# Optimization experiments

Hardware: AMD Instinct MI355X
Metric: run time of the kernel (lower is better)

The kernel has to match this reference:

```python
import jax, jax.numpy as jnp
import numpy as np

B, C, H, W = 32, 256, 64, 64
M, D = 256, 512           # memory_size, memory_dim
NH, HD = 8, 64            # heads, head_dim
EPS = 1e-5


def setup_inputs() -> dict:
    key = jax.random.key(0)
    ks = jax.random.split(key, 12)
    s = 0.02
    return {
        "x": jax.random.normal(ks[0], (B, C, H, W), jnp.float32),
        "memory_bank": jax.random.normal(ks[1], (M, D), jnp.float32),
        "enc_conv_w": jax.random.normal(ks[2], (D // 2, C), jnp.float32) * s,  # 1x1 conv == channel matmul
        "enc_conv_b": jnp.zeros((D // 2,), jnp.float32),
        "bn_gamma": jnp.ones((D // 2,), jnp.float32),
        "bn_beta": jnp.zeros((D // 2,), jnp.float32),
        "bn_mean": jnp.zeros((D // 2,), jnp.float32),
        "bn_var": jnp.ones((D // 2,), jnp.float32),
        "enc_lin_w": jax.random.normal(ks[3], (D, D // 2), jnp.float32) * s,
        "enc_lin_b": jnp.zeros((D,), jnp.float32),
        "ln_gamma": jnp.ones((D,), jnp.float32),
        "ln_beta": jnp.zeros((D,), jnp.float32),
        "attn_in_w": jax.random.normal(ks[4], (3 * D, D), jnp.float32) * s,
        "attn_in_b": jnp.zeros((3 * D,), jnp.float32),
        "attn_out_w": jax.random.normal(ks[5], (D, D), jnp.float32) * s,
        "attn_out_b": jnp.zeros((D,), jnp.float32),
        "gate_w": jax.random.normal(ks[6], (D, 2 * D), jnp.float32) * s,
        "gate_b": jnp.zeros((D,), jnp.float32),
        "rec_w1": jax.random.normal(ks[7], (D // 2, D), jnp.float32) * s,
        "rec_b1": jnp.zeros((D // 2,), jnp.float32),
        "rec_w2": jax.random.normal(ks[8], (C, D // 2), jnp.float32) * s,
        "rec_b2": jnp.zeros((C,), jnp.float32),
        "spat_conv_w": jax.random.normal(ks[9], (1, 2, 7, 7), jnp.float32) * s,
    }


def reference(x, memory_bank, enc_conv_w, enc_conv_b, bn_gamma, bn_beta, bn_mean, bn_var,
              enc_lin_w, enc_lin_b, ln_gamma, ln_beta, attn_in_w, attn_in_b,
              attn_out_w, attn_out_b, gate_w, gate_b, rec_w1, rec_b1, rec_w2, rec_b2,
              spat_conv_w):
    # ---- feature encoder: 1x1 conv -> BN(eval) -> ReLU -> global avg pool -> Linear -> LayerNorm ----
    h = jnp.einsum('bchw,oc->bohw', x, enc_conv_w) + enc_conv_b[None, :, None, None]
    bn_scale = (bn_gamma / jnp.sqrt(bn_var + EPS))[None, :, None, None]
    h = (h - bn_mean[None, :, None, None]) * bn_scale + bn_beta[None, :, None, None]
    h = jax.nn.relu(h)
    h = h.mean(axis=(2, 3))                                   # (B, D//2)
    h = h @ enc_lin_w.T + enc_lin_b                           # (B, D)
    mu = h.mean(-1, keepdims=True)
    var = h.var(-1, keepdims=True)
    enc = (h - mu) / jnp.sqrt(var + EPS) * ln_gamma + ln_beta  # (B, D)

    # ---- memory retrieval: MHA with q_len=1, keys/values = shared memory bank ----
    Wq, Wk, Wv = jnp.split(attn_in_w, 3, axis=0)
    bq, bk, bv = jnp.split(attn_in_b, 3)
    q = (enc @ Wq.T + bq).reshape(B, NH, HD)                  # (B, H, d)
    k = (memory_bank @ Wk.T + bk).reshape(M, NH, HD)          # (M, H, d) — batch-shared
    v = (memory_bank @ Wv.T + bv).reshape(M, NH, HD)
    scores = jnp.einsum('bhd,mhd->bhm', q, k) / np.float32(np.sqrt(HD))
    att = jax.nn.softmax(scores, axis=-1)                     # (B, H, M)
    ctx = jnp.einsum('bhm,mhd->bhd', att, v).reshape(B, D)
    retrieved = ctx @ attn_out_w.T + attn_out_b               # (B, D)

    # ---- gated fusion ----
    gate = jax.nn.sigmoid(jnp.concatenate([enc, retrieved], axis=-1) @ gate_w.T + gate_b)
    fused = gate * enc + (1.0 - gate) * retrieved             # (B, D)

    # ---- per-channel weights from fused features ----
    sw = jax.nn.sigmoid(jax.nn.relu(fused @ rec_w1.T + rec_b1) @ rec_w2.T + rec_b2)  # (B, C)

    # ---- spatial attention on [avg, max] channel stats ----
    avg = x.mean(axis=1, keepdims=True)
    mx = x.max(axis=1, keepdims=True)
    sp_in = jnp.concatenate([avg, mx], axis=1)                # (B, 2, H, W)
    sa = jax.lax.conv_general_dilated(sp_in, spat_conv_w, (1, 1), [(3, 3), (3, 3)],
                                      dimension_numbers=('NCHW', 'OIHW', 'NCHW'))
    sa = jax.nn.sigmoid(sa)                                   # (B, 1, H, W)

    return x * sw[:, :, None, None] * sa                      # (B, C, H, W)
```

## Files before the change

### kernel.cpp

```cpp
#include <hip/hip_runtime.h>
#include <math.h>

#define EPSV 1e-5f

typedef __attribute__((ext_vector_type(8))) short short8;
typedef __attribute__((ext_vector_type(8))) unsigned short ushort8;
typedef __attribute__((ext_vector_type(4))) float f32x4;

__device__ __forceinline__ unsigned short f2bf(float f){
  unsigned u = __builtin_bit_cast(unsigned, f);
  u += 0x7fffu + ((u >> 16) & 1u);
  return (unsigned short)(u >> 16);
}
__device__ __forceinline__ float dot4f(float4 w, const float* v){
  return w.x*v[0] + w.y*v[1] + w.z*v[2] + w.w*v[3];
}
__device__ __forceinline__ float sigmoidf(float v){ return 1.f/(1.f + expf(-v)); }

__global__ __launch_bounds__(256) void k_pack(const float* __restrict__ w1,
                                              const float* __restrict__ wattn,
                                              unsigned short* __restrict__ p1,
                                              unsigned short* __restrict__ pkv){
  const int total1 = 256*256, total2 = 1024*512;
  for (int idx = blockIdx.x*256 + threadIdx.x; idx < total1 + total2; idx += gridDim.x*256){
    if (idx < total1){
      int o = idx >> 8, c = idx & 255;
      int off = (((o>>4)*8 + (c>>5))*64 + (((c>>3)&3)*16 + (o&15)))*8 + (c&7);
      p1[off] = f2bf(w1[idx]);
    } else {
      int j = idx - total1; int o = j >> 9, c = j & 511;
      int off = (((o>>4)*16 + (c>>5))*64 + (((c>>3)&3)*16 + (o&15)))*8 + (c&7);
      pkv[off] = f2bf(wattn[512*512 + j]);
    }
  }
}

__global__ __launch_bounds__(256) void k_conv(
    const float* __restrict__ x, const unsigned short* __restrict__ wp,
    const float* __restrict__ cb, const float* __restrict__ bng,
    const float* __restrict__ bnb, const float* __restrict__ bnm,
    const float* __restrict__ bnv,
    float* __restrict__ ppool, float* __restrict__ wavg, float* __restrict__ wmax){
  int bid = blockIdx.x;
  int b = bid >> 6, tile = bid & 63;
  int px0 = tile << 6;
  int t = threadIdx.x;
  int lane = t & 63, wv = t >> 6;
  int px = t & 63, cg = wv;
  __shared__ __align__(16) unsigned short a_lds[16384];
  __shared__ float st_s[256], st_m[256];

  const float* xb = x + (size_t)b*(256*4096) + px0 + px;

  float ssum = 0.f, smax = -3.4e38f;
  const unsigned wbase = (((px >> 4) << 6) + ((unsigned)cg << 4) + (px & 15)) << 4;

  #pragma unroll
  for (int ch = 0; ch < 8; ++ch){
    float xv[8];
    #pragma unroll
    for (int u = 0; u < 8; ++u)
      xv[u] = xb[(size_t)(ch*32 + cg*8 + u) * 4096];
    ushort8 pk;
    #pragma unroll
    for (int u = 0; u < 8; ++u){
      ssum += xv[u];
      smax = fmaxf(smax, xv[u]);
      pk[u] = f2bf(xv[u]);
    }
    *(ushort8*)((char*)a_lds + wbase + (ch << 12)) = pk;
  }
  st_s[t] = ssum; st_m[t] = smax;
  __syncthreads();

  if (t < 64){
    float s = st_s[t] + st_s[t+64] + st_s[t+128] + st_s[t+192];
    float m = fmaxf(fmaxf(st_m[t], st_m[t+64]), fmaxf(st_m[t+128], st_m[t+192]));
    wavg[(b << 12) + px0 + t] = s * (1.f/256.f);
    wmax[(b << 12) + px0 + t] = m;
  }

  f32x4 acc[4][4];
  #pragma unroll
  for (int i = 0; i < 4; ++i)
    #pragma unroll
    for (int j = 0; j < 4; ++j){ f32x4 z = {0.f,0.f,0.f,0.f}; acc[i][j] = z; }

  #pragma unroll
  for (int ch = 0; ch < 8; ++ch){
    short8 afr[4];
    #pragma unroll
    for (int mf = 0; mf < 4; ++mf)
      afr[mf] = *(const short8*)((const char*)a_lds + (ch << 12) + (mf << 10) + lane*16);
    #pragma unroll
    for (int nf = 0; nf < 4; ++nf){
      short8 bfr = *(const short8*)(wp + (size_t)(((wv*4 + nf)*8 + ch) * 512 + lane*8));
      #pragma unroll
      for (int mf = 0; mf < 4; ++mf)
        acc[mf][nf] = __builtin_amdgcn_mfma_f32_16x16x32_bf16(afr[mf], bfr, acc[mf][nf], 0, 0, 0);
    }
  }

  #pragma unroll
  for (int nf = 0; nf < 4; ++nf){
    int o = (wv << 6) + (nf << 4) + (lane & 15);
    float sc = bng[o] * rsqrtf(bnv[o] + EPSV);
    float sh = bnb[o] + (cb[o] - bnm[o]) * sc;
    float ps = 0.f;
    #pragma unroll
    for (int mf = 0; mf < 4; ++mf)
      #pragma unroll
      for (int r = 0; r < 4; ++r)
        ps += fmaxf(acc[mf][nf][r] * sc + sh, 0.f);
    ps += __shfl_xor(ps, 16, 64);
    ps += __shfl_xor(ps, 32, 64);
    if ((lane & 48) == 0)
      ppool[(size_t)((b << 6) + tile)*256 + o] = ps;
  }
}

__global__ __launch_bounds__(256) void k_enc(const float* __restrict__ pp,
    const float* __restrict__ lw, const float* __restrict__ lb,
    const float* __restrict__ lng, const float* __restrict__ lnb,
    float* __restrict__ enc){
  int b = blockIdx.x, t = threadIdx.x;
  __shared__ __align__(16) float p_s[256];
  __shared__ float h_s[512], red[8];
  float s = 0.f;
  for (int tile = 0; tile < 64; ++tile) s += pp[(size_t)((b<<6)+tile)*256 + t];
  p_s[t] = s * (1.f/4096.f);
  __syncthreads();
  float hv[2];
  #pragma unroll
  for (int k = 0; k < 2; ++k){
    int d = t + k*256;
    const float4* wr = (const float4*)(lw + (size_t)d*256);
    float a = 0.f;
    for (int j = 0; j < 64; ++j) a += dot4f(wr[j], &p_s[4*j]);
    hv[k] = a + lb[d];
    h_s[d] = hv[k];
  }
  float ls = hv[0] + hv[1], lq = hv[0]*hv[0] + hv[1]*hv[1];
  #pragma unroll
  for (int msk = 1; msk < 64; msk <<= 1){
    ls += __shfl_xor(ls, msk, 64);
    lq += __shfl_xor(lq, msk, 64);
  }
  if ((t & 63) == 0){ red[t>>6] = ls; red[4 + (t>>6)] = lq; }
  __syncthreads();
  float su = red[0]+red[1]+red[2]+red[3];
  float sq = red[4]+red[5]+red[6]+red[7];
  float mu = su * (1.f/512.f);
  float vr = sq * (1.f/512.f) - mu*mu;
  float rstd = rsqrtf(vr + EPSV);
  #pragma unroll
  for (int k = 0; k < 2; ++k){
    int d = t + k*256;
    enc[(size_t)b*512 + d] = (h_s[d] - mu)*rstd*lng[d] + lnb[d];
  }
}

__global__ __launch_bounds__(256) void k_kv(const float* __restrict__ mb,
    const unsigned short* __restrict__ wp, const float* __restrict__ attb,
    float* __restrict__ kvb){
  int bid = blockIdx.x;
  int mt = bid >> 4, nt = bid & 15;
  int m0 = mt << 4;
  int mu = nt >> 3;
  int ncol0 = (nt & 7) << 6;
  int t = threadIdx.x, lane = t & 63, wv = t >> 6;
  int l15 = lane & 15, l4 = lane >> 4;

  const float* arow = mb + (size_t)(m0 + l15)*512 + l4*8;
  int ofrag = (nt << 2) + wv;

  f32x4 acc = {0.f,0.f,0.f,0.f};
  #pragma unroll
  for (int ch = 0; ch < 16; ++ch){
    float4 a0 = *(const float4*)(arow + ch*32);
    float4 a1 = *(const float4*)(arow + ch*32 + 4);
    short8 afr;
    afr[0] = (short)f2bf(a0.x); afr[1] = (short)f2bf(a0.y);
    afr[2] = (short)f2bf(a0.z); afr[3] = (short)f2bf(a0.w);
    afr[4] = (short)f2bf(a1.x); afr[5] = (short)f2bf(a1.y);
    afr[6] = (short)f2bf(a1.z); afr[7] = (short)f2bf(a1.w);
    short8 bfr = *(const short8*)(wp + (size_t)(ofrag*16 + ch)*512 + lane*8);
    acc = __builtin_amdgcn_mfma_f32_16x16x32_bf16(afr, bfr, acc, 0, 0, 0);
  }
  float bias = attb[512 + mu*512 + ncol0 + (wv << 4) + l15];
  #pragma unroll
  for (int i = 0; i < 4; ++i){
    int row = m0 + l4*4 + i;
    int col = ncol0 + (wv << 4) + l15;
    kvb[(size_t)mu*131072 + (size_t)row*512 + col] = acc[i] + bias;
  }
}

__global__ __launch_bounds__(256) void k_qkattn(const float* __restrict__ enc,
    const float* __restrict__ kvb, const float* __restrict__ attw,
    const float* __restrict__ attb, float* __restrict__ ctxout){
  int bid = blockIdx.x;
  int b = bid >> 3, h = bid & 7;
  int t = threadIdx.x;
  __shared__ float e_s[512];
  __shared__ __align__(16) float q_s[64];
  __shared__ float att_s[256];
  __shared__ float red_s[256];
  __shared__ float r2[8];

  e_s[t]       = enc[(size_t)b*512 + t];
  e_s[t + 256] = enc[(size_t)b*512 + 256 + t];
  __syncthreads();

  {
    int i = t >> 2, part = t & 3;
    const float4* wr = (const float4*)(attw + (size_t)(h*64 + i)*512 + part*128);
    const float* ev = e_s + part*128;
    float a = 0.f;
    #pragma unroll
    for (int j = 0; j < 32; ++j) a += dot4f(wr[j], ev + 4*j);
    a += __shfl_xor(a, 1, 64);
    a += __shfl_xor(a, 2, 64);
    if (part == 0) q_s[i] = a + attb[h*64 + i];
  }
  __syncthreads();

  float sc;
  {
    const float4* kr = (const float4*)(kvb + (size_t)t*512 + h*64);
    const float4* qr = (const float4*)q_s;
    float a = 0.f;
    #pragma unroll
    for (int j = 0; j < 16; ++j){
      float4 kk = kr[j], qq = qr[j];
      a += kk.x*qq.x + kk.y*qq.y + kk.z*qq.z + kk.w*qq.w;
    }
    sc = a * 0.125f;
  }
  int wv = t >> 6, lane = t & 63;
  float mx = sc;
  #pragma unroll
  for (int msk = 1; msk < 64; msk <<= 1) mx = fmaxf(mx, __shfl_xor(mx, msk, 64));
  if (lane == 0) r2[wv] = mx;
  __syncthreads();
  mx = fmaxf(fmaxf(r2[0], r2[1]), fmaxf(r2[2], r2[3]));
  float ex = expf(sc - mx);
  float sum = ex;
  #pragma unroll
  for (int msk = 1; msk < 64; msk <<= 1) sum += __shfl_xor(sum, msk, 64);
  if (lane == 0) r2[4 + wv] = sum;
  __syncthreads();
  float inv = 1.f / (r2[4] + r2[5] + r2[6] + r2[7]);
  att_s[t] = ex * inv;
  __syncthreads();

  {
    const float* vbase = kvb + 131072 + (size_t)(wv*64)*512 + h*64 + lane;
    const float* at = att_s + wv*64;
    float a = 0.f;
    #pragma unroll 8
    for (int m = 0; m < 64; ++m) a += at[m] * vbase[(size_t)m*512];
    red_s[wv*64 + lane] = a;
  }
  __syncthreads();
  if (t < 64)
    ctxout[(size_t)b*512 + h*64 + t] = red_s[t] + red_s[64+t] + red_s[128+t] + red_s[192+t];
}

__global__ __launch_bounds__(256) void k_outproj(const float* __restrict__ ctx,
    const float* __restrict__ ow, const float* __restrict__ obv,
    float* __restrict__ retr){
  int bid = blockIdx.x;
  int b = bid >> 3, n0 = (bid & 7) << 6;
  int t = threadIdx.x;
  __shared__ float c_s[512];
  c_s[t]       = ctx[(size_t)b*512 + t];
  c_s[t + 256] = ctx[(size_t)b*512 + 256 + t];
  __syncthreads();
  int o = n0 + (t >> 2), part = t & 3;
  const float4* wr = (const float4*)(ow + (size_t)o*512 + part*128);
  const float* cv = c_s + part*128;
  float a = 0.f;
  #pragma unroll
  for (int j = 0; j < 32; ++j) a += dot4f(wr[j], cv + 4*j);
  a += __shfl_xor(a, 1, 64);
  a += __shfl_xor(a, 2, 64);
  if (part == 0) retr[(size_t)b*512 + o] = a + obv[o];
}

__global__ __launch_bounds__(256) void k_gate(const float* __restrict__ enc,
    const float* __restrict__ retr, const float* __restrict__ gw,
    const float* __restrict__ gb, float* __restrict__ fused){
  int bid = blockIdx.x;
  int b = bid >> 3, n0 = (bid & 7) << 6;
  int t = threadIdx.x;
  __shared__ float ef[1024];
  ef[t]        = enc[(size_t)b*512 + t];
  ef[t + 256]  = enc[(size_t)b*512 + 256 + t];
  ef[t + 512]  = retr[(size_t)b*512 + t];
  ef[t + 768]  = retr[(size_t)b*512 + 256 + t];
  __syncthreads();
  int o = n0 + (t >> 2), part = t & 3;
  const float4* wr = (const float4*)(gw + (size_t)o*1024 + part*256);
  const float* fv = ef + part*256;
  float a = 0.f;
  #pragma unroll
  for (int j = 0; j < 64; ++j) a += dot4f(wr[j], fv + 4*j);
  a += __shfl_xor(a, 1, 64);
  a += __shfl_xor(a, 2, 64);
  if (part == 0){
    float g = sigmoidf(a + gb[o]);
    fused[(size_t)b*512 + o] = g*ef[o] + (1.f - g)*ef[512 + o];
  }
}

__global__ __launch_bounds__(256) void k_rec1(const float* __restrict__ fused,
    const float* __restrict__ r1w, const float* __restrict__ r1b,
    float* __restrict__ t1){
  int bid = blockIdx.x;
  int b = bid >> 2, n0 = (bid & 3) << 6;
  int t = threadIdx.x;
  __shared__ float f_s[512];
  f_s[t]       = fused[(size_t)b*512 + t];
  f_s[t + 256] = fused[(size_t)b*512 + 256 + t];
  __syncthreads();
  int o = n0 + (t >> 2), part = t & 3;
  const float4* wr = (const float4*)(r1w + (size_t)o*512 + part*128);
  const float* fv = f_s + part*128;
  float a = 0.f;
  #pragma unroll
  for (int j = 0; j < 32; ++j) a += dot4f(wr[j], fv + 4*j);
  a += __shfl_xor(a, 1, 64);
  a += __shfl_xor(a, 2, 64);
  if (part == 0) t1[(size_t)b*256 + o] = fmaxf(a + r1b[o], 0.f);
}

__global__ __launch_bounds__(256) void k_rec2(const float* __restrict__ t1,
    const float* __restrict__ r2w, const float* __restrict__ r2b,
    float* __restrict__ swout){
  int bid = blockIdx.x;
  int b = bid >> 2, n0 = (bid & 3) << 6;
  int t = threadIdx.x;
  __shared__ float t_s[256];
  t_s[t] = t1[(size_t)b*256 + t];
  __syncthreads();
  int o = n0 + (t >> 2), part = t & 3;
  const float4* wr = (const float4*)(r2w + (size_t)o*256 + part*64);
  const float* tv = t_s + part*64;
  float a = 0.f;
  #pragma unroll
  for (int j = 0; j < 16; ++j) a += dot4f(wr[j], tv + 4*j);
  a += __shfl_xor(a, 1, 64);
  a += __shfl_xor(a, 2, 64);
  if (part == 0) swout[(size_t)b*256 + o] = sigmoidf(a + r2b[o]);
}

__global__ __launch_bounds__(256) void k_spconv(const float* __restrict__ wavg,
    const float* __restrict__ wmax, const float* __restrict__ wgt,
    float* __restrict__ sa){
  __shared__ float w_s[98];
  int t = threadIdx.x;
  if (t < 98) w_s[t] = wgt[t];
  __syncthreads();
  int b = blockIdx.x >> 4;
  int px = ((blockIdx.x & 15) << 8) + t;
  int y = px >> 6, xx = px & 63;
  const float* pa = wavg + (b << 12);
  const float* pm = wmax + (b << 12);
  float a = 0.f;
  #pragma unroll
  for (int ky = 0; ky < 7; ++ky){
    int yy = y + ky - 3;
    if (yy < 0 || yy >= 64) continue;
    #pragma unroll
    for (int kx = 0; kx < 7; ++kx){
      int x2 = xx + kx - 3;
      if (x2 < 0 || x2 >= 64) continue;
      int o = (yy << 6) + x2;
      a += pa[o]*w_s[ky*7+kx] + pm[o]*w_s[49+ky*7+kx];
    }
  }
  sa[(b << 12) + px] = sigmoidf(a);
}

__global__ __launch_bounds__(256) void k_final(const float* __restrict__ x,
    const float* __restrict__ sw, const float* __restrict__ sa,
    float* __restrict__ out){
  const size_t total = 8388608;
  for (size_t q = (size_t)blockIdx.x*256 + threadIdx.x; q < total; q += (size_t)gridDim.x*256){
    size_t b = q >> 18;
    int c = (int)((q >> 10) & 255);
    int p4 = (int)(q & 1023);
    float4 xv = ((const float4*)x)[q];
    float4 sv = ((const float4*)sa)[(b << 10) + p4];
    float s = sw[(b << 8) + c];
    float4 o;
    o.x = xv.x * s * sv.x;
    o.y = xv.y * s * sv.y;
    o.z = xv.z * s * sv.z;
    o.w = xv.w * s * sv.w;
    ((float4*)out)[q] = o;
  }
}

extern "C" void kernel_launch(void* const* d_in, const int* in_sizes, int n_in,
                              void* d_out, int out_size, void* d_ws, size_t ws_size,
                              hipStream_t stream){
  const float* x    = (const float*)d_in[0];
  const float* mb   = (const float*)d_in[1];
  const float* w1   = (const float*)d_in[2];
  const float* cbv  = (const float*)d_in[3];
  const float* bng  = (const float*)d_in[4];
  const float* bnb  = (const float*)d_in[5];
  const float* bnm  = (const float*)d_in[6];
  const float* bnv  = (const float*)d_in[7];
  const float* lw   = (const float*)d_in[8];
  const float* lb   = (const float*)d_in[9];
  const float* lng  = (const float*)d_in[10];
  const float* lnb  = (const float*)d_in[11];
  const float* attw = (const float*)d_in[12];
  const float* attb = (const float*)d_in[13];
  const float* ow   = (const float*)d_in[14];
  const float* obv  = (const float*)d_in[15];
  const float* gw   = (const float*)d_in[16];
  const float* gb   = (const float*)d_in[17];
  const float* r1w  = (const float*)d_in[18];
  const float* r1b  = (const float*)d_in[19];
  const float* r2w  = (const float*)d_in[20];
  const float* r2b  = (const float*)d_in[21];
  const float* spw  = (const float*)d_in[22];
  float* out = (float*)d_out;

  char* ws = (char*)d_ws;
  unsigned short* w1p  = (unsigned short*)(ws + 0);
  unsigned short* wkvp = (unsigned short*)(ws + 131072);
  float* ppool = (float*)(ws + 1179648);
  float* wavg  = (float*)(ws + 3276800);
  float* wmax  = (float*)(ws + 3801088);
  float* encb  = (float*)(ws + 4325376);
  float* kvb   = (float*)(ws + 4390912);
  float* swb   = (float*)(ws + 5439488);
  float* sab   = (float*)(ws + 5472256);
  float* ctxb  = (float*)(ws + 5996544);
  float* retrb = (float*)(ws + 6062080);
  float* fusedb= (float*)(ws + 6127616);
  float* t1b   = (float*)(ws + 6193152);

  k_pack   <<<2304, 256, 0, stream>>>(w1, attw, w1p, wkvp);
  k_conv   <<<2048, 256, 0, stream>>>(x, w1p, cbv, bng, bnb, bnm, bnv, ppool, wavg, wmax);
  k_enc    <<<32,   256, 0, stream>>>(ppool, lw, lb, lng, lnb, encb);
  k_kv     <<<256,  256, 0, stream>>>(mb, wkvp, attb, kvb);
  k_qkattn <<<256,  256, 0, stream>>>(encb, kvb, attw, attb, ctxb);
  k_outproj<<<256,  256, 0, stream>>>(ctxb, ow, obv, retrb);
  k_gate   <<<256,  256, 0, stream>>>(encb, retrb, gw, gb, fusedb);
  k_rec1   <<<128,  256, 0, stream>>>(fusedb, r1w, r1b, t1b);
  k_rec2   <<<128,  256, 0, stream>>>(t1b, r2w, r2b, swb);
  k_spconv <<<512,  256, 0, stream>>>(wavg, wmax, spw, sab);
  k_final  <<<2048, 256, 0, stream>>>(x, swb, sab, out);
}
```

Measured before the change: 179.3 us.

## Restructure conv GEMM with larger tiles, double-buffered LDS and prefetched loads

The 1x1-conv kernel now processes 256 pixels per block with 512 threads arranged as a 2x4 wave grid, instead of 64 pixels per 256-thread block. The channel dimension is streamed in 32-channel chunks through a double-buffered, XOR-swizzled LDS stage, and the next chunk's float4 global loads are issued before the MFMAs on the current chunk. This is meant to overlap global loads with matrix math, widen loads to float4, and reduce LDS bank conflicts and the number of partial pools. In exchange it uses more registers per thread (32 accumulator tiles) and launches only 512 blocks, which may lower occupancy. The partial-pool count per batch falls from 64 to 16, and the encoder reduction is updated to match.

```diff
diff --git a/kernel.cpp b/kernel.cpp
--- a/kernel.cpp
+++ b/kernel.cpp
@@ -5,6 +5,7 @@
 
 typedef __attribute__((ext_vector_type(8))) short short8;
 typedef __attribute__((ext_vector_type(8))) unsigned short ushort8;
+typedef __attribute__((ext_vector_type(4))) unsigned short ushort4v;
 typedef __attribute__((ext_vector_type(4))) float f32x4;
 
 __device__ __forceinline__ unsigned short f2bf(float f){
@@ -35,88 +36,116 @@
   }
 }
 
-__global__ __launch_bounds__(256) void k_conv(
+__global__ __launch_bounds__(512, 2) void k_conv(
     const float* __restrict__ x, const unsigned short* __restrict__ wp,
     const float* __restrict__ cb, const float* __restrict__ bng,
     const float* __restrict__ bnb, const float* __restrict__ bnm,
     const float* __restrict__ bnv,
     float* __restrict__ ppool, float* __restrict__ wavg, float* __restrict__ wmax){
   int bid = blockIdx.x;
-  int b = bid >> 6, tile = bid & 63;
-  int px0 = tile << 6;
+  int b = bid >> 4, tile = bid & 15;
+  int px0 = tile << 8;
   int t = threadIdx.x;
   int lane = t & 63, wv = t >> 6;
-  int px = t & 63, cg = wv;
-  __shared__ __align__(16) unsigned short a_lds[16384];
-  __shared__ float st_s[256], st_m[256];
-
-  const float* xb = x + (size_t)b*(256*4096) + px0 + px;
-
-  float ssum = 0.f, smax = -3.4e38f;
-  const unsigned wbase = (((px >> 4) << 6) + ((unsigned)cg << 4) + (px & 15)) << 4;
-
-  #pragma unroll
-  for (int ch = 0; ch < 8; ++ch){
-    float xv[8];
-    #pragma unroll
-    for (int u = 0; u < 8; ++u)
-      xv[u] = xb[(size_t)(ch*32 + cg*8 + u) * 4096];
-    ushort8 pk;
-    #pragma unroll
-    for (int u = 0; u < 8; ++u){
-      ssum += xv[u];
-      smax = fmaxf(smax, xv[u]);
-      pk[u] = f2bf(xv[u]);
-    }
-    *(ushort8*)((char*)a_lds + wbase + (ch << 12)) = pk;
-  }
-  st_s[t] = ssum; st_m[t] = smax;
-  __syncthreads();
-
-  if (t < 64){
-    float s = st_s[t] + st_s[t+64] + st_s[t+128] + st_s[t+192];
-    float m = fmaxf(fmaxf(st_m[t], st_m[t+64]), fmaxf(st_m[t+128], st_m[t+192]));
+  int wm = wv >> 2, wn = wv & 3;
+
+  __shared__ __align__(16) unsigned short a_lds[2][8192];
+  __shared__ float st_s[8][256];
+  __shared__ float sm_s[8][256];
+  __shared__ float pr_s[2][256];
+
+  const float* xb = x + (size_t)b*(256*4096) + px0;
+
+  float ss[4] = {0.f,0.f,0.f,0.f};
+  float smx[4] = {-3.4e38f,-3.4e38f,-3.4e38f,-3.4e38f};
+
+  f32x4 acc[8][4];
+  #pragma unroll
+  for (int m = 0; m < 8; ++m)
+    #pragma unroll
+    for (int n = 0; n < 4; ++n){ f32x4 z = {0.f,0.f,0.f,0.f}; acc[m][n] = z; }
+
+  unsigned wb[4];
+  const int g = (wv >> 1) & 3, jh = wv & 1;
+  #pragma unroll
+  for (int i = 0; i < 4; ++i){
+    int px = 4*lane + i;
+    unsigned byte = (unsigned)((px >> 6) << 12) + ((unsigned)((px >> 4) & 3) << 10)
+                  + ((unsigned)g << 8) + ((unsigned)(px & 15) << 4) + ((unsigned)jh << 3);
+    wb[i] = byte ^ (((unsigned)(px >> 4) & 7u) << 4);
+  }
+
+  float4 ld[4];
+  #pragma unroll
+  for (int q = 0; q < 4; ++q)
+    ld[q] = *(const float4*)(xb + (size_t)(wv*4 + q)*4096 + lane*4);
+
+  for (int kc = 0; kc < 8; ++kc){
+    if (kc > 0) __syncthreads();
+    char* stg = (char*)a_lds[kc & 1];
+    #pragma unroll
+    for (int i = 0; i < 4; ++i){
+      float v0 = ld[0][i], v1 = ld[1][i], v2 = ld[2][i], v3 = ld[3][i];
+      ss[i] += (v0 + v1) + (v2 + v3);
+      smx[i] = fmaxf(fmaxf(smx[i], fmaxf(v0, v1)), fmaxf(v2, v3));
+      ushort4v pk;
+      pk[0] = f2bf(v0); pk[1] = f2bf(v1); pk[2] = f2bf(v2); pk[3] = f2bf(v3);
+      *(ushort4v*)(stg + wb[i]) = pk;
+    }
+    if (kc < 7){
+      #pragma unroll
+      for (int q = 0; q < 4; ++q)
+        ld[q] = *(const float4*)(xb + (size_t)((kc+1)*32 + wv*4 + q)*4096 + lane*4);
+    }
+    __syncthreads();
+    const char* rd = (const char*)a_lds[kc & 1];
+    short8 afr[8];
+    #pragma unroll
+    for (int m = 0; m < 8; ++m){
+      int pxb = wm*128 + m*16;
+      unsigned byte = (unsigned)((pxb >> 6) << 12) + ((unsigned)(m & 3) << 10)
+                    + ((unsigned)(lane >> 4) << 8) + ((unsigned)(lane & 15) << 4);
+      afr[m] = *(const short8*)(rd + (byte ^ ((unsigned)(m & 7) << 4)));
+    }
+    #pragma unroll
+    for (int nf = 0; nf < 4; ++nf){
+      short8 bfr = *(const short8*)(wp + (size_t)(((wn*4 + nf)*8 + kc) * 512 + lane*8));
+      #pragma unroll
+      for (int m = 0; m < 8; ++m)
+        acc[m][nf] = __builtin_amdgcn_mfma_f32_16x16x32_bf16(afr[m], bfr, acc[m][nf], 0, 0, 0);
+    }
+  }
+
+  *(float4*)&st_s[wv][4*lane] = *(float4*)ss;
+  *(float4*)&sm_s[wv][4*lane] = *(float4*)smx;
+  __syncthreads();
+  if (t < 256){
+    float s = 0.f, m = -3.4e38f;
+    #pragma unroll
+    for (int w = 0; w < 8; ++w){ s += st_s[w][t]; m = fmaxf(m, sm_s[w][t]); }
     wavg[(b << 12) + px0 + t] = s * (1.f/256.f);
     wmax[(b << 12) + px0 + t] = m;
   }
 
-  f32x4 acc[4][4];
-  #pragma unroll
-  for (int i = 0; i < 4; ++i)
-    #pragma unroll
-    for (int j = 0; j < 4; ++j){ f32x4 z = {0.f,0.f,0.f,0.f}; acc[i][j] = z; }
-
-  #pragma unroll
-  for (int ch = 0; ch < 8; ++ch){
-    short8 afr[4];
-    #pragma unroll
-    for (int mf = 0; mf < 4; ++mf)
-      afr[mf] = *(const short8*)((const char*)a_lds + (ch << 12) + (mf << 10) + lane*16);
-    #pragma unroll
-    for (int nf = 0; nf < 4; ++nf){
-      short8 bfr = *(const short8*)(wp + (size_t)(((wv*4 + nf)*8 + ch) * 512 + lane*8));
-      #pragma unroll
-      for (int mf = 0; mf < 4; ++mf)
-        acc[mf][nf] = __builtin_amdgcn_mfma_f32_16x16x32_bf16(afr[mf], bfr, acc[mf][nf], 0, 0, 0);
-    }
-  }
-
   #pragma unroll
   for (int nf = 0; nf < 4; ++nf){
-    int o = (wv << 6) + (nf << 4) + (lane & 15);
+    int o = (wn << 6) + (nf << 4) + (lane & 15);
     float sc = bng[o] * rsqrtf(bnv[o] + EPSV);
     float sh = bnb[o] + (cb[o] - bnm[o]) * sc;
     float ps = 0.f;
     #pragma unroll
-    for (int mf = 0; mf < 4; ++mf)
+    for (int m = 0; m < 8; ++m)
       #pragma unroll
       for (int r = 0; r < 4; ++r)
-        ps += fmaxf(acc[mf][nf][r] * sc + sh, 0.f);
+        ps += fmaxf(acc[m][nf][r] * sc + sh, 0.f);
     ps += __shfl_xor(ps, 16, 64);
     ps += __shfl_xor(ps, 32, 64);
     if ((lane & 48) == 0)
-      ppool[(size_t)((b << 6) + tile)*256 + o] = ps;
-  }
+      pr_s[wm][(wn << 6) + (nf << 4) + lane] = ps;
+  }
+  __syncthreads();
+  if (t < 256)
+    ppool[(size_t)((b << 4) + tile)*256 + t] = pr_s[0][t] + pr_s[1][t];
 }
 
 __global__ __launch_bounds__(256) void k_enc(const float* __restrict__ pp,
@@ -127,7 +156,7 @@
   __shared__ __align__(16) float p_s[256];
   __shared__ float h_s[512], red[8];
   float s = 0.f;
-  for (int tile = 0; tile < 64; ++tile) s += pp[(size_t)((b<<6)+tile)*256 + t];
+  for (int tile = 0; tile < 16; ++tile) s += pp[(size_t)((b<<4)+tile)*256 + t];
   p_s[t] = s * (1.f/4096.f);
   __syncthreads();
   float hv[2];
@@ -447,7 +476,7 @@
   float* t1b   = (float*)(ws + 6193152);
 
   k_pack   <<<2304, 256, 0, stream>>>(w1, attw, w1p, wkvp);
-  k_conv   <<<2048, 256, 0, stream>>>(x, w1p, cbv, bng, bnb, bnm, bnv, ppool, wavg, wmax);
+  k_conv   <<<512,  512, 0, stream>>>(x, w1p, cbv, bng, bnb, bnm, bnv, ppool, wavg, wmax);
   k_enc    <<<32,   256, 0, stream>>>(ppool, lw, lb, lng, lnb, encb);
   k_kv     <<<256,  256, 0, stream>>>(mb, wkvp, attb, kvb);
   k_qkattn <<<256,  256, 0, stream>>>(encb, kvb, attw, attb, ctxb);
```

Result: no change. 181.9 us (median of 4 runs) (+1.4%).

## Split conv into bf16 transpose pass and larger-tile MFMA GEMM kernel

Applied to the files above, without the earlier changes.

Replaces the fused conv kernel, which read x with channel-strided scalar loads, with two kernels. The first converts x to bf16 and writes it in an MFMA-fragment layout using coalesced float4 loads and an LDS transpose. The second is a 512-thread GEMM over 128-pixel tiles that computes the avg/max channel stats from the bf16 copy and reduces the partial pools in LDS, halving the ppool entries. This adds an extra round trip through global memory for a 64 MB bf16 intermediate. The spatial stats are now computed from bf16-rounded values, so avg and max lose some precision.

```diff
diff --git a/kernel.cpp b/kernel.cpp
--- a/kernel.cpp
+++ b/kernel.cpp
@@ -11,6 +11,9 @@
   unsigned u = __builtin_bit_cast(unsigned, f);
   u += 0x7fffu + ((u >> 16) & 1u);
   return (unsigned short)(u >> 16);
+}
+__device__ __forceinline__ float bf2f(unsigned short u){
+  return __builtin_bit_cast(float, ((unsigned)u) << 16);
 }
 __device__ __forceinline__ float dot4f(float4 w, const float* v){
   return w.x*v[0] + w.y*v[1] + w.z*v[2] + w.w*v[3];
@@ -35,50 +38,61 @@
   }
 }
 
-__global__ __launch_bounds__(256) void k_conv(
-    const float* __restrict__ x, const unsigned short* __restrict__ wp,
+__global__ __launch_bounds__(512) void k_xpose(const float* __restrict__ x,
+                                               unsigned short* __restrict__ xa){
+  int bid = blockIdx.x;
+  int b = bid >> 5, cg = bid & 31;
+  int t = threadIdx.x;
+  __shared__ unsigned int lds[12288];
+  const float* base = x + (size_t)b*1048576 + (size_t)cg*32768;
+  unsigned short* xab = xa + (size_t)b*1048576;
+
+  for (int half = 0; half < 2; ++half){
+    if (half) __syncthreads();
+    int px0 = half*2048;
+    #pragma unroll
+    for (int u = 0; u < 4; ++u){
+      float4 a = *(const float4*)(base + (size_t)(2*u)*4096 + px0 + 4*t);
+      float4 c = *(const float4*)(base + (size_t)(2*u+1)*4096 + px0 + 4*t);
+      float av[4] = {a.x, a.y, a.z, a.w};
+      float cv[4] = {c.x, c.y, c.z, c.w};
+      #pragma unroll
+      for (int i = 0; i < 4; ++i)
+        lds[(4*t + i)*6 + u] = (unsigned)f2bf(av[i]) | ((unsigned)f2bf(cv[i]) << 16);
+    }
+    __syncthreads();
+    #pragma unroll
+    for (int k = 0; k < 4; ++k){
+      int p = k*512 + t;
+      int PX = px0 + p;
+      uint2 q0 = *(const uint2*)(&lds[p*6]);
+      uint2 q1 = *(const uint2*)(&lds[p*6 + 2]);
+      uint4 val; val.x = q0.x; val.y = q0.y; val.z = q1.x; val.w = q1.y;
+      size_t off = ((size_t)((PX >> 8)*128 + (cg >> 2)*16 + ((PX >> 4) & 15)) << 9)
+                 + ((unsigned)(cg & 3) << 7) + ((unsigned)(PX & 15) << 3);
+      *(uint4*)(xab + off) = val;
+    }
+  }
+}
+
+__global__ __launch_bounds__(512, 4) void k_gemm(
+    const unsigned short* __restrict__ xa, const unsigned short* __restrict__ wp,
     const float* __restrict__ cb, const float* __restrict__ bng,
     const float* __restrict__ bnb, const float* __restrict__ bnm,
     const float* __restrict__ bnv,
     float* __restrict__ ppool, float* __restrict__ wavg, float* __restrict__ wmax){
   int bid = blockIdx.x;
-  int b = bid >> 6, tile = bid & 63;
-  int px0 = tile << 6;
-  int t = threadIdx.x;
-  int lane = t & 63, wv = t >> 6;
-  int px = t & 63, cg = wv;
+  int b = bid >> 5, pt2 = bid & 31;
+  int pt = pt2 >> 1, half = pt2 & 1;
+  int t = threadIdx.x, lane = t & 63, wv = t >> 6;
+  int wm = wv >> 2, wn = wv & 3;
   __shared__ __align__(16) unsigned short a_lds[16384];
-  __shared__ float st_s[256], st_m[256];
-
-  const float* xb = x + (size_t)b*(256*4096) + px0 + px;
-
+  __shared__ float pr_s[2][256];
+
+  const unsigned short* src = xa + (size_t)b*1048576 + (size_t)pt*65536
+                                 + (size_t)half*4096;
+  int px = t >> 2, q = t & 3;
   float ssum = 0.f, smax = -3.4e38f;
-  const unsigned wbase = (((px >> 4) << 6) + ((unsigned)cg << 4) + (px & 15)) << 4;
-
-  #pragma unroll
-  for (int ch = 0; ch < 8; ++ch){
-    float xv[8];
-    #pragma unroll
-    for (int u = 0; u < 8; ++u)
-      xv[u] = xb[(size_t)(ch*32 + cg*8 + u) * 4096];
-    ushort8 pk;
-    #pragma unroll
-    for (int u = 0; u < 8; ++u){
-      ssum += xv[u];
-      smax = fmaxf(smax, xv[u]);
-      pk[u] = f2bf(xv[u]);
-    }
-    *(ushort8*)((char*)a_lds + wbase + (ch << 12)) = pk;
-  }
-  st_s[t] = ssum; st_m[t] = smax;
-  __syncthreads();
-
-  if (t < 64){
-    float s = st_s[t] + st_s[t+64] + st_s[t+128] + st_s[t+192];
-    float m = fmaxf(fmaxf(st_m[t], st_m[t+64]), fmaxf(st_m[t+128], st_m[t+192]));
-    wavg[(b << 12) + px0 + t] = s * (1.f/256.f);
-    wmax[(b << 12) + px0 + t] = m;
-  }
 
   f32x4 acc[4][4];
   #pragma unroll
@@ -86,24 +100,53 @@
     #pragma unroll
     for (int j = 0; j < 4; ++j){ f32x4 z = {0.f,0.f,0.f,0.f}; acc[i][j] = z; }
 
-  #pragma unroll
-  for (int ch = 0; ch < 8; ++ch){
-    short8 afr[4];
-    #pragma unroll
-    for (int mf = 0; mf < 4; ++mf)
-      afr[mf] = *(const short8*)((const char*)a_lds + (ch << 12) + (mf << 10) + lane*16);
-    #pragma unroll
-    for (int nf = 0; nf < 4; ++nf){
-      short8 bfr = *(const short8*)(wp + (size_t)(((wv*4 + nf)*8 + ch) * 512 + lane*8));
+  for (int s = 0; s < 2; ++s){
+    if (s) __syncthreads();
+    #pragma unroll
+    for (int r = 0; r < 4; ++r){
+      ushort8 v = *(const ushort8*)(src + (size_t)(s*4 + r)*8192 + t*8);
+      *(ushort8*)(a_lds + r*4096 + t*8) = v;
+    }
+    __syncthreads();
+    #pragma unroll
+    for (int c = 0; c < 4; ++c){
+      ushort8 sv = *(const ushort8*)(a_lds + ((c*8 + (px >> 4)) << 9)
+                                           + ((q*16 + (px & 15)) << 3));
+      #pragma unroll
+      for (int j = 0; j < 8; ++j){
+        float f = bf2f(sv[j]);
+        ssum += f; smax = fmaxf(smax, f);
+      }
+    }
+    #pragma unroll
+    for (int kcl = 0; kcl < 4; ++kcl){
+      short8 afr[4];
       #pragma unroll
       for (int mf = 0; mf < 4; ++mf)
-        acc[mf][nf] = __builtin_amdgcn_mfma_f32_16x16x32_bf16(afr[mf], bfr, acc[mf][nf], 0, 0, 0);
-    }
+        afr[mf] = *(const short8*)(a_lds + ((kcl*8 + wm*4 + mf) << 9) + lane*8);
+      #pragma unroll
+      for (int nf = 0; nf < 4; ++nf){
+        short8 bfr = *(const short8*)(wp + (size_t)(((wn*4 + nf)*8 + s*4 + kcl)*512) + lane*8);
+        #pragma unroll
+        for (int mf = 0; mf < 4; ++mf)
+          acc[mf][nf] = __builtin_amdgcn_mfma_f32_16x16x32_bf16(afr[mf], bfr, acc[mf][nf], 0, 0, 0);
+      }
+    }
+  }
+
+  ssum += __shfl_xor(ssum, 1, 64);
+  ssum += __shfl_xor(ssum, 2, 64);
+  smax = fmaxf(smax, __shfl_xor(smax, 1, 64));
+  smax = fmaxf(smax, __shfl_xor(smax, 2, 64));
+  if (q == 0){
+    int PX = pt2*128 + px;
+    wavg[(b << 12) + PX] = ssum * (1.f/256.f);
+    wmax[(b << 12) + PX] = smax;
   }
 
   #pragma unroll
   for (int nf = 0; nf < 4; ++nf){
-    int o = (wv << 6) + (nf << 4) + (lane & 15);
+    int o = (wn << 6) + (nf << 4) + (lane & 15);
     float sc = bng[o] * rsqrtf(bnv[o] + EPSV);
     float sh = bnb[o] + (cb[o] - bnm[o]) * sc;
     float ps = 0.f;
@@ -115,8 +158,11 @@
     ps += __shfl_xor(ps, 16, 64);
     ps += __shfl_xor(ps, 32, 64);
     if ((lane & 48) == 0)
-      ppool[(size_t)((b << 6) + tile)*256 + o] = ps;
-  }
+      pr_s[wm][(wn << 6) + (nf << 4) + lane] = ps;
+  }
+  __syncthreads();
+  if (t < 256)
+    ppool[(size_t)((b << 5) + pt2)*256 + t] = pr_s[0][t] + pr_s[1][t];
 }
 
 __global__ __launch_bounds__(256) void k_enc(const float* __restrict__ pp,
@@ -127,7 +173,7 @@
   __shared__ __align__(16) float p_s[256];
   __shared__ float h_s[512], red[8];
   float s = 0.f;
-  for (int tile = 0; tile < 64; ++tile) s += pp[(size_t)((b<<6)+tile)*256 + t];
+  for (int tile = 0; tile < 32; ++tile) s += pp[(size_t)((b<<5)+tile)*256 + t];
   p_s[t] = s * (1.f/4096.f);
   __syncthreads();
   float hv[2];
@@ -445,9 +491,11 @@
   float* retrb = (float*)(ws + 6062080);
   float* fusedb= (float*)(ws + 6127616);
   float* t1b   = (float*)(ws + 6193152);
+  unsigned short* xa = (unsigned short*)(ws + 8388608);
 
   k_pack   <<<2304, 256, 0, stream>>>(w1, attw, w1p, wkvp);
-  k_conv   <<<2048, 256, 0, stream>>>(x, w1p, cbv, bng, bnb, bnm, bnv, ppool, wavg, wmax);
+  k_xpose  <<<1024, 512, 0, stream>>>(x, xa);
+  k_gemm   <<<1024, 512, 0, stream>>>(xa, w1p, cbv, bng, bnb, bnm, bnv, ppool, wavg, wmax);
   k_enc    <<<32,   256, 0, stream>>>(ppool, lw, lb, lng, lnb, encb);
   k_kv     <<<256,  256, 0, stream>>>(mb, wkvp, attb, kvb);
   k_qkattn <<<256,  256, 0, stream>>>(encb, kvb, attw, attb, ctxb);
```

Result: slower. 214.2 us (+19.4%).
